# Optimization experiments

Hardware: AMD Instinct MI355X
Metric: run time of the kernel (lower is better)

The kernel has to match this reference:

```python
import jax, jax.numpy as jnp
import numpy as np

# Straight-through sign binarization (BinaryNet semantics: .data mutation => identity grad)
@jax.custom_vjp
def binarize(x):
    return jnp.sign(x)

def _bin_fwd(x):
    return jnp.sign(x), None

def _bin_bwd(res, g):
    return (g,)

binarize.defvjp(_bin_fwd, _bin_bwd)

def hardtanh(x):
    return jnp.clip(x, -1.0, 1.0)

def bconv2d(x, w, stride):
    # binarize both input and weight, VALID conv, NCHW/OIHW
    return jax.lax.conv_general_dilated(
        binarize(x), binarize(w),
        window_strides=(stride, stride), padding='VALID',
        dimension_numbers=('NCHW', 'OIHW', 'NCHW'))

def blinear(x, w):
    # binarize input and weight; w is [out, in]
    return binarize(x) @ binarize(w).T

def setup_inputs() -> dict:
    key = jax.random.key(0)
    ks = jax.random.split(key, 6)
    B = 131072
    return {
        'x':    jax.random.normal(ks[0], (B, 1, 15, 15), dtype=jnp.float32),
        'w1':   jax.random.normal(ks[1], (4, 1, 3, 3),  dtype=jnp.float32),
        'w2':   jax.random.normal(ks[2], (8, 4, 3, 3),  dtype=jnp.float32),
        'w3':   jax.random.normal(ks[3], (16, 8, 3, 3), dtype=jnp.float32),
        'wfc1': jax.random.normal(ks[4], (8, 16),       dtype=jnp.float32),
        'wfc2': jax.random.normal(ks[5], (1, 8),        dtype=jnp.float32),
    }

def reference(x, w1, w2, w3, wfc1, wfc2):
    out = hardtanh(bconv2d(x, w1, 2))        # [B,4,7,7]
    out = hardtanh(bconv2d(out, w2, 2))      # [B,8,3,3]
    out = hardtanh(bconv2d(out, w3, 2))      # [B,16,1,1]
    out = out.reshape(-1, 16)                # [B,16]
    out = hardtanh(blinear(out, wfc1))       # [B,8]
    out = blinear(out, wfc2)                 # [B,1]
    return out
```

## Files before the change

kernel.cpp:

```cpp
#include <hip/hip_runtime.h>
#include <stdint.h>

typedef uint32_t u32;
typedef uint64_t u64;


__global__ __launch_bounds__(64, 2) void binnet(const float* __restrict__ x,
                                                const float* __restrict__ w1,
                                                const float* __restrict__ w2,
                                                const float* __restrict__ w3,
                                                const float* __restrict__ wfc1,
                                                const float* __restrict__ wfc2,
                                                float* __restrict__ out) {
  __shared__ u64 st[228];
  const int lane = threadIdx.x;
  const int b0 = blockIdx.x * 64;

  const float* xw = x + (size_t)b0 * 225 + lane;
  if (lane < 3) st[225 + lane] = 0;
  #pragma unroll
  for (int g = 0; g < 5; ++g) {
    float v[45];
    #pragma unroll
    for (int k = 0; k < 45; ++k) v[k] = xw[(g * 45 + k) * 64];
    #pragma unroll
    for (int k = 0; k < 45; ++k) {
      const u64 m = __ballot(v[k] < 0.f);
      if (lane == 0) st[g * 45 + k] = m;
    }
  }

  const float vw1 = w1[lane < 36 ? lane : 0];
  const u64 m1 = __ballot((lane < 36) && (vw1 < 0.f));
  const u32 w1p0 = (u32)(m1      ) & 0x1FFu;
  const u32 w1p1 = (u32)(m1 >>  9) & 0x1FFu;
  const u32 w1p2 = (u32)(m1 >> 18) & 0x1FFu;
  const u32 w1p3 = (u32)(m1 >> 27) & 0x1FFu;

  const int w2i = (lane < 36) ? ((lane & 3) * 9 + (lane >> 2)) : 0;
  u64 W2[8];
  #pragma unroll
  for (int d = 0; d < 8; ++d) {
    const float v = w2[d * 36 + w2i];
    W2[d] = __ballot((lane < 36) && (v < 0.f));
  }

  const int w3i = (lane & 7) * 9 + (lane >> 3);
  u64 W3L[16];
  u32 W3H[16];
  #pragma unroll
  for (int e = 0; e < 16; ++e) W3L[e] = __ballot(w3[e * 72 + w3i] < 0.f);
  {
    const int hb = (lane & 7) * 9 + 8;
    const u64 h0 = __ballot(w3[((lane >> 3)    ) * 72 + hb] < 0.f);
    const u64 h1 = __ballot(w3[((lane >> 3) + 8) * 72 + hb] < 0.f);
    #pragma unroll
    for (int e = 0; e < 16; ++e)
      W3H[e] = (u32)(((e < 8 ? h0 : h1) >> (8 * (e & 7))) & 0xFFu);
  }

  const u64 f0 = __ballot(wfc1[lane] < 0.f);
  const u64 f1 = __ballot(wfc1[64 + lane] < 0.f);
  u32 WF1[8];
  #pragma unroll
  for (int j = 0; j < 8; ++j)
    WF1[j] = (u32)(((j < 4 ? f0 : f1) >> (16 * (j & 3))) & 0xFFFFu);

  const float vf2 = wfc2[lane < 8 ? lane : 0];
  const u32 wf2 = (u32)__ballot((lane < 8) && (vf2 < 0.f)) & 0xFFu;

  __syncthreads();

  const u64* stw = st;
  const int f0i = 225 * lane;
  const int w0 = f0i >> 6;
  const int sh = f0i & 63;
  u64 Wd[5];
  #pragma unroll
  for (int i = 0; i < 5; ++i) Wd[i] = stw[w0 + i];
  u64 Bv[4];
  #pragma unroll
  for (int i = 0; i < 4; ++i)
    Bv[i] = (Wd[i] >> sh) | ((Wd[i + 1] << (63 - sh)) << 1);

  u32 rb[15];
  #pragma unroll
  for (int r = 0; r < 15; ++r) {
    const int f = 15 * r, w = f >> 6, o = f & 63;
    u64 v = Bv[w] >> o;
    if (o > 49) v |= Bv[w + 1] << (64 - o);
    rb[r] = (u32)v & 0x7FFFu;
  }

  u64 a1[4] = {0, 0, 0, 0};
  int pix = 0;
  #pragma unroll
  for (int oy = 0; oy < 7; ++oy) {
    const u32 r0 = rb[2 * oy], r1 = rb[2 * oy + 1], r2 = rb[2 * oy + 2];
    #pragma unroll
    for (int ox = 0; ox < 7; ++ox) {
      const u32 t9 = ((r0 >> (2 * ox)) & 7) | (((r1 >> (2 * ox)) & 7) << 3)
                   | (((r2 >> (2 * ox)) & 7) << 6);
      u32 nib = 0;
      nib |= (u32)(__popc(t9 ^ w1p0) >= 5) << 0;
      nib |= (u32)(__popc(t9 ^ w1p1) >= 5) << 1;
      nib |= (u32)(__popc(t9 ^ w1p2) >= 5) << 2;
      nib |= (u32)(__popc(t9 ^ w1p3) >= 5) << 3;
      a1[pix >> 4] |= (u64)nib << ((pix & 15) * 4);
      ++pix;
    }
  }

  u64 v2lo = 0, nz2lo = 0; u32 v2hi = 0, nz2hi = 0;
  #pragma unroll
  for (int oy = 0; oy < 3; ++oy) {
    #pragma unroll
    for (int ox = 0; ox < 3; ++ox) {
      u64 T = 0;
      #pragma unroll
      for (int ky = 0; ky < 3; ++ky) {
        const int p = 4 * (7 * (2 * oy + ky) + 2 * ox);
        const int w = p >> 6, o = p & 63;
        u64 v = a1[w] >> o;
        if (o > 52) v |= a1[w + 1] << (64 - o);
        T |= (v & 0xFFFull) << (12 * ky);
      }
      const int pix2 = 3 * oy + ox;
      u32 bv = 0, bz = 0;
      #pragma unroll
      for (int d = 0; d < 8; ++d) {
        const int cnt = __popcll(T ^ W2[d]);
        bv |= (u32)(cnt > 18) << d;
        bz |= (u32)(cnt != 18) << d;
      }
      if (pix2 < 8) { v2lo |= (u64)bv << (8 * pix2); nz2lo |= (u64)bz << (8 * pix2); }
      else          { v2hi = bv; nz2hi = bz; }
    }
  }

  const int nztot = __popcll(nz2lo) + __popc(nz2hi);
  u32 s3v = 0, s3nz = 0;
  #pragma unroll
  for (int e = 0; e < 16; ++e) {
    const int cnt = __popcll(nz2lo & (v2lo ^ W3L[e])) + __popc(nz2hi & (v2hi ^ W3H[e]));
    const int s = nztot - 2 * cnt;
    s3v  |= (u32)(s < 0) << e;
    s3nz |= (u32)(s != 0) << e;
  }

  const int n3 = __popc(s3nz);
  u32 hv = 0, hz = 0;
  #pragma unroll
  for (int j = 0; j < 8; ++j) {
    const int c2 = __popc(s3nz & (s3v ^ WF1[j]));
    const int s = n3 - 2 * c2;
    hv |= (u32)(s < 0) << j;
    hz |= (u32)(s != 0) << j;
  }

  const int c3 = __popc(hz & (hv ^ wf2));
  const int sfin = __popc(hz) - 2 * c3;
  out[b0 + lane] = (float)sfin;
}

extern "C" void kernel_launch(void* const* d_in, const int* in_sizes, int n_in,
                              void* d_out, int out_size, void* d_ws, size_t ws_size,
                              hipStream_t stream) {
  const float* x    = (const float*)d_in[0];
  const float* w1   = (const float*)d_in[1];
  const float* w2   = (const float*)d_in[2];
  const float* w3   = (const float*)d_in[3];
  const float* wfc1 = (const float*)d_in[4];
  const float* wfc2 = (const float*)d_in[5];
  float* out = (float*)d_out;
  const int B = in_sizes[0] / 225;

  (void)d_ws; (void)ws_size; (void)n_in; (void)out_size;
  binnet<<<B / 64, 64, 0, stream>>>(x, w1, w2, w3, wfc1, wfc2, out);
}
```

Before: 185.5 us.

## Load input as float4 and rebuild flat sign bitmask via bit-interleave in LDS

Input is now loaded with 128-bit float4 loads instead of scalar loads. Each component gets its own ballot into a component-planar shared buffer, and a bit-spreading pass interleaves the four planes back into the flat per-sample bit layout. This cuts the number of global load instructions and should make memory access wider. The cost is an extra shared-memory pass, an added barrier and more ALU work for the bit spreading.

```diff
diff --git a/kernel.cpp b/kernel.cpp
--- a/kernel.cpp
+++ b/kernel.cpp
@@ -4,6 +4,24 @@
 typedef uint32_t u32;
 typedef uint64_t u64;
 
+
+__device__ __forceinline__ u64 spread4(u64 x) {
+  x &= 0xFFFFull;
+  x = (x | (x << 24)) & 0x000000FF000000FFull;
+  x = (x | (x << 12)) & 0x000F000F000F000Full;
+  x = (x | (x <<  6)) & 0x0303030303030303ull;
+  x = (x | (x <<  3)) & 0x1111111111111111ull;
+  return x;
+}
+
+__device__ __forceinline__ u64 flat_from(const u64* stP, int w) {
+  const int t4 = (w >> 2) << 2;
+  const int q = (w & 3) * 16;
+  return  spread4(stP[t4 + 0] >> q)
+       | (spread4(stP[t4 + 1] >> q) << 1)
+       | (spread4(stP[t4 + 2] >> q) << 2)
+       | (spread4(stP[t4 + 3] >> q) << 3);
+}
 
 __global__ __launch_bounds__(64, 2) void binnet(const float* __restrict__ x,
                                                 const float* __restrict__ w1,
@@ -12,23 +30,49 @@
                                                 const float* __restrict__ wfc1,
                                                 const float* __restrict__ wfc2,
                                                 float* __restrict__ out) {
-  __shared__ u64 st[228];
+  __shared__ u64 stP[224];
+  __shared__ u64 stF[228];
   const int lane = threadIdx.x;
   const int b0 = blockIdx.x * 64;
 
-  const float* xw = x + (size_t)b0 * 225 + lane;
-  if (lane < 3) st[225 + lane] = 0;
-  #pragma unroll
-  for (int g = 0; g < 5; ++g) {
-    float v[45];
-    #pragma unroll
-    for (int k = 0; k < 45; ++k) v[k] = xw[(g * 45 + k) * 64];
-    #pragma unroll
-    for (int k = 0; k < 45; ++k) {
-      const u64 m = __ballot(v[k] < 0.f);
-      if (lane == 0) st[g * 45 + k] = m;
+  const float* xw = x + (size_t)b0 * 225;
+  const float4* xq = (const float4*)xw;
+  if (lane < 3) stF[225 + lane] = 0;
+  #pragma unroll
+  for (int g = 0; g < 4; ++g) {
+    float4 v[14];
+    #pragma unroll
+    for (int k = 0; k < 14; ++k) v[k] = xq[(g * 14 + k) * 64 + lane];
+    #pragma unroll
+    for (int k = 0; k < 14; ++k) {
+      const int T = g * 14 + k;
+      const u64 m0 = __ballot(v[k].x < 0.f);
+      const u64 m1 = __ballot(v[k].y < 0.f);
+      const u64 m2 = __ballot(v[k].z < 0.f);
+      const u64 m3 = __ballot(v[k].w < 0.f);
+      if (lane == 0) {
+        stP[4 * T + 0] = m0; stP[4 * T + 1] = m1;
+        stP[4 * T + 2] = m2; stP[4 * T + 3] = m3;
+      }
     }
   }
+  {
+    const float tv = xw[14336 + lane];
+    const u64 m = __ballot(tv < 0.f);
+    if (lane == 0) stF[224] = m;
+  }
+  __syncthreads();
+
+  #pragma unroll
+  for (int k = 0; k < 3; ++k) {
+    const int w = lane + 64 * k;
+    stF[w] = flat_from(stP, w);
+  }
+  if (lane < 32) {
+    const int w = 192 + lane;
+    stF[w] = flat_from(stP, w);
+  }
+  __syncthreads();
 
   const float vw1 = w1[lane < 36 ? lane : 0];
   const u64 m1 = __ballot((lane < 36) && (vw1 < 0.f));
@@ -59,19 +103,17 @@
       W3H[e] = (u32)(((e < 8 ? h0 : h1) >> (8 * (e & 7))) & 0xFFu);
   }
 
-  const u64 f0 = __ballot(wfc1[lane] < 0.f);
-  const u64 f1 = __ballot(wfc1[64 + lane] < 0.f);
+  const u64 f0b = __ballot(wfc1[lane] < 0.f);
+  const u64 f1b = __ballot(wfc1[64 + lane] < 0.f);
   u32 WF1[8];
   #pragma unroll
   for (int j = 0; j < 8; ++j)
-    WF1[j] = (u32)(((j < 4 ? f0 : f1) >> (16 * (j & 3))) & 0xFFFFu);
+    WF1[j] = (u32)(((j < 4 ? f0b : f1b) >> (16 * (j & 3))) & 0xFFFFu);
 
   const float vf2 = wfc2[lane < 8 ? lane : 0];
   const u32 wf2 = (u32)__ballot((lane < 8) && (vf2 < 0.f)) & 0xFFu;
 
-  __syncthreads();
-
-  const u64* stw = st;
+  const u64* stw = stF;
   const int f0i = 225 * lane;
   const int w0 = f0i >> 6;
   const int sh = f0i & 63;
```

Result: no change. 187.6 us (+1.1%).

## Load each sample's input directly per thread with float4 and drop shared staging

Applied to the files above, without the earlier changes.

Each thread now reads its own 225-float sample with float4 loads (57 vectors, using the misaligned offset) and packs sign bits into registers, instead of the block loading coalesced floats, ballot-packing them into shared memory, and each lane re-extracting its bits. This removes the ballots, shared-memory traffic and the barrier. In exchange, accesses are strided per lane (900-byte stride between lanes), so coalescing is poorer and it relies on L2/L1 to absorb the scattered loads. It also reads up to 3 floats past the end of the last sample, which may be out of bounds for the final thread.

```diff
diff --git a/kernel.cpp b/kernel.cpp
--- a/kernel.cpp
+++ b/kernel.cpp
@@ -12,22 +12,49 @@
                                                 const float* __restrict__ wfc1,
                                                 const float* __restrict__ wfc2,
                                                 float* __restrict__ out) {
-  __shared__ u64 st[228];
   const int lane = threadIdx.x;
-  const int b0 = blockIdx.x * 64;
+  const int gid = blockIdx.x * 64 + lane;
+  const int f0 = gid * 225;
+  const int q0 = f0 >> 2;
+  const int off = f0 & 3;
+  const float4* xq = (const float4*)x + q0;
 
-  const float* xw = x + (size_t)b0 * 225 + lane;
-  if (lane < 3) st[225 + lane] = 0;
+  u64 SW[4] = {0, 0, 0, 0};
   #pragma unroll
-  for (int g = 0; g < 5; ++g) {
-    float v[45];
+  for (int g = 0; g < 4; ++g) {
+    float4 v[14];
     #pragma unroll
-    for (int k = 0; k < 45; ++k) v[k] = xw[(g * 45 + k) * 64];
+    for (int k = 0; k < 14; ++k) v[k] = xq[g * 14 + k];
     #pragma unroll
-    for (int k = 0; k < 45; ++k) {
-      const u64 m = __ballot(v[k] < 0.f);
-      if (lane == 0) st[g * 45 + k] = m;
+    for (int k = 0; k < 14; ++k) {
+      const int rel = (g * 14 + k) * 4;
+      SW[(rel    ) >> 6] |= (u64)(v[k].x < 0.f) << ((rel    ) & 63);
+      SW[(rel + 1) >> 6] |= (u64)(v[k].y < 0.f) << ((rel + 1) & 63);
+      SW[(rel + 2) >> 6] |= (u64)(v[k].z < 0.f) << ((rel + 2) & 63);
+      SW[(rel + 3) >> 6] |= (u64)(v[k].w < 0.f) << ((rel + 3) & 63);
     }
+  }
+  {
+    const float4 v = xq[56];
+    SW[3] |= (u64)(v.x < 0.f) << 32;
+    SW[3] |= (u64)(v.y < 0.f) << 33;
+    SW[3] |= (u64)(v.z < 0.f) << 34;
+    SW[3] |= (u64)(v.w < 0.f) << 35;
+  }
+
+  u64 Bv[4];
+  Bv[0] = (SW[0] >> off) | ((SW[1] << (63 - off)) << 1);
+  Bv[1] = (SW[1] >> off) | ((SW[2] << (63 - off)) << 1);
+  Bv[2] = (SW[2] >> off) | ((SW[3] << (63 - off)) << 1);
+  Bv[3] = (SW[3] >> off) & 0x1FFFFFFFFull;
+
+  u32 rb[15];
+  #pragma unroll
+  for (int r = 0; r < 15; ++r) {
+    const int f = 15 * r, w = f >> 6, o = f & 63;
+    u64 v = Bv[w] >> o;
+    if (o > 49) v |= Bv[w + 1] << (64 - o);
+    rb[r] = (u32)v & 0x7FFFu;
   }
 
   const float vw1 = w1[lane < 36 ? lane : 0];
@@ -59,38 +86,15 @@
       W3H[e] = (u32)(((e < 8 ? h0 : h1) >> (8 * (e & 7))) & 0xFFu);
   }
 
-  const u64 f0 = __ballot(wfc1[lane] < 0.f);
-  const u64 f1 = __ballot(wfc1[64 + lane] < 0.f);
+  const u64 f0b = __ballot(wfc1[lane] < 0.f);
+  const u64 f1b = __ballot(wfc1[64 + lane] < 0.f);
   u32 WF1[8];
   #pragma unroll
   for (int j = 0; j < 8; ++j)
-    WF1[j] = (u32)(((j < 4 ? f0 : f1) >> (16 * (j & 3))) & 0xFFFFu);
+    WF1[j] = (u32)(((j < 4 ? f0b : f1b) >> (16 * (j & 3))) & 0xFFFFu);
 
   const float vf2 = wfc2[lane < 8 ? lane : 0];
   const u32 wf2 = (u32)__ballot((lane < 8) && (vf2 < 0.f)) & 0xFFu;
-
-  __syncthreads();
-
-  const u64* stw = st;
-  const int f0i = 225 * lane;
-  const int w0 = f0i >> 6;
-  const int sh = f0i & 63;
-  u64 Wd[5];
-  #pragma unroll
-  for (int i = 0; i < 5; ++i) Wd[i] = stw[w0 + i];
-  u64 Bv[4];
-  #pragma unroll
-  for (int i = 0; i < 4; ++i)
-    Bv[i] = (Wd[i] >> sh) | ((Wd[i + 1] << (63 - sh)) << 1);
-
-  u32 rb[15];
-  #pragma unroll
-  for (int r = 0; r < 15; ++r) {
-    const int f = 15 * r, w = f >> 6, o = f & 63;
-    u64 v = Bv[w] >> o;
-    if (o > 49) v |= Bv[w + 1] << (64 - o);
-    rb[r] = (u32)v & 0x7FFFu;
-  }
 
   u64 a1[4] = {0, 0, 0, 0};
   int pix = 0;
@@ -160,7 +164,7 @@
 
   const int c3 = __popc(hz & (hv ^ wf2));
   const int sfin = __popc(hz) - 2 * c3;
-  out[b0 + lane] = (float)sfin;
+  out[gid] = (float)sfin;
 }
 
 extern "C" void kernel_launch(void* const* d_in, const int* in_sizes, int n_in,
```

After: 192.7 us. 3.8% more time.
